# Optimization experiments

Measured on AMD Instinct MI355X. Metric: run time of the kernel, lower is better.

## Reference

```python
import jax, jax.numpy as jnp
import numpy as np

N_NODES = 10000
N_EDGES = 320000
ND, ED = 256, 128
CAT = 2 * ND + ED  # 640


def setup_inputs() -> dict:
    key = jax.random.key(0)
    ks = jax.random.split(key, 12)
    s = 0.05
    inp = {
        'node_attr': jax.random.normal(ks[0], (N_NODES, ND), jnp.float32),
        'edge_attr': jax.random.normal(ks[1], (N_EDGES, ED), jnp.float32),
        'edge_index': jax.random.randint(ks[2], (2, N_EDGES), 0, N_NODES, jnp.int32),
        'mw0': jax.random.normal(ks[3], (CAT, ND), jnp.float32) * s,
        'mb0': jnp.zeros((ND,), jnp.float32),
        'mw1': jax.random.normal(ks[4], (ND, ND), jnp.float32) * s,
        'mb1': jnp.zeros((ND,), jnp.float32),
        'mw2': jax.random.normal(ks[5], (ND, ND), jnp.float32) * s,
        'mb2': jnp.zeros((ND,), jnp.float32),
        'ew0': jax.random.normal(ks[6], (CAT, ED), jnp.float32) * s,
        'eb0': jnp.zeros((ED,), jnp.float32),
        'ew1': jax.random.normal(ks[7], (ED, ED), jnp.float32) * s,
        'eb1': jnp.zeros((ED,), jnp.float32),
        'ew2': jax.random.normal(ks[8], (ED, ED), jnp.float32) * s,
        'eb2': jnp.zeros((ED,), jnp.float32),
        'aw': jax.random.normal(ks[9], (CAT, 1), jnp.float32) * s,
        'ab': jnp.zeros((1,), jnp.float32),
    }
    return inp


def _mlp3(f, w0, b0, w1, b1, w2, b2):
    h = jax.nn.relu(f @ w0 + b0)
    h = jax.nn.relu(h @ w1 + b1)
    return h @ w2 + b2


def reference(node_attr, edge_attr, edge_index,
              mw0, mb0, mw1, mb1, mw2, mb2,
              ew0, eb0, ew1, eb1, ew2, eb2, aw, ab):
    n = node_attr.shape[0]
    src, dst = edge_index[0], edge_index[1]
    # [E, 2*ND+ED] gathered per-edge features
    feat = jnp.concatenate([node_attr[src], node_attr[dst], edge_attr], axis=-1)

    messages = _mlp3(feat, mw0, mb0, mw1, mb1, mw2, mb2)        # [E, ND]
    att = (feat @ aw + ab)[:, 0]                                 # [E]

    # scatter_softmax over edges grouped by source node (stable)
    seg_max = jax.ops.segment_max(att, src, num_segments=n)
    seg_max = jnp.where(jnp.isfinite(seg_max), seg_max, 0.0)     # empty segments
    ex = jnp.exp(att - seg_max[src])
    denom = jax.ops.segment_sum(ex, src, num_segments=n)
    alpha = ex / denom[src]                                      # [E]

    x_out = jax.ops.segment_sum(alpha[:, None] * messages, src, num_segments=n)  # [N, ND]
    e_out = _mlp3(feat, ew0, eb0, ew1, eb1, ew2, eb2)            # [E, ED]
    return x_out, e_out
```

## Files before the change

kernel.cpp:

```cpp
#include <hip/hip_runtime.h>
#include <hip/hip_bf16.h>

#define N_NODES 10000
#define E_EDGES 320000
#define ND 256
#define ED 128

#define B_AM   0
#define B_BM   5120000
#define B_AE   10240000
#define B_BE   12800000
#define B_P1   15360000
#define B_P2   15400960
#define B_XA   15441920
#define B_DEN  25681920
#define B_CNT  25722880
#define B_ROW  25763840
#define B_CUR  25804800
#define B_EID  25845760
#define B_WT   27125760

#define M0T 0
#define M1T 65536
#define M2T 196608
#define E0T 327680
#define E1T 360448
#define E2T 393216

#define R0 0
#define R1 16384
#define R2 32768
#define R3 49152
#define AL_S  65536
#define SRC_S 65792
#define DST_S 66048
#define EID_S 66304
#define LDS_TOT 66560

#define BM 64
#define NTILES (E_EDGES / BM)

typedef float  float4v __attribute__((ext_vector_type(4)));
typedef short  short8  __attribute__((ext_vector_type(8)));

__device__ __forceinline__ unsigned short f2bf(float f) {
    unsigned int b = __float_as_uint(f);
    return (unsigned short)((b + 0x7FFFu + ((b >> 16) & 1u)) >> 16);
}
__device__ __forceinline__ float bf2f(unsigned short u) {
    return __uint_as_float(((unsigned int)u) << 16);
}
__device__ __forceinline__ unsigned int pkbf(float a, float b) {
    __hip_bfloat162 h = __float22bfloat162_rn(float2{a, b});
    return *(unsigned int*)&h;
}

__device__ __forceinline__ void bar_ldsonly() {
    asm volatile("s_waitcnt lgkmcnt(0)" ::: "memory");
    __builtin_amdgcn_s_barrier();
}

__global__ void k_init(float* xa, float* den, int* cnt, int* cur) {
    int i = blockIdx.x * blockDim.x + threadIdx.x;
    int st = gridDim.x * blockDim.x;
    for (int j = i; j < N_NODES * ND; j += st) xa[j] = 0.f;
    for (int j = i; j < N_NODES; j += st) { den[j] = 0.f; cnt[j] = 0; cur[j] = 0; }
}

__global__ void k_deg(const int* ei, int* cnt) {
    int e = blockIdx.x * 256 + threadIdx.x;
    if (e < E_EDGES) atomicAdd(&cnt[ei[e]], 1);
}

__global__ __launch_bounds__(1024) void k_scan(const int* cnt, int* rowstart) {
    __shared__ int wsum[16];
    int t = threadIdx.x, lane = t & 63, w = t >> 6;
    int base = t * 10;
    int loc[10];
    int s = 0;
    #pragma unroll
    for (int i = 0; i < 10; i++) {
        int idx = base + i;
        int v = (idx < N_NODES) ? cnt[idx] : 0;
        loc[i] = s; s += v;
    }
    int run = s;
    #pragma unroll
    for (int d = 1; d < 64; d <<= 1) {
        int u = __shfl_up(run, d);
        if (lane >= d) run += u;
    }
    if (lane == 63) wsum[w] = run;
    __syncthreads();
    if (w == 0 && lane < 16) {
        int v = wsum[lane];
        int r = v;
        #pragma unroll
        for (int d = 1; d < 16; d <<= 1) {
            int u = __shfl_up(r, d);
            if (lane >= d) r += u;
        }
        wsum[lane] = r - v;
    }
    __syncthreads();
    int ex = wsum[w] + run - s;
    #pragma unroll
    for (int i = 0; i < 10; i++) {
        int idx = base + i;
        if (idx < N_NODES) rowstart[idx] = ex + loc[i];
    }
}

__global__ void k_fill(const int* ei, const int* rowstart, int* cur, int* eidcsr) {
    int e = blockIdx.x * 256 + threadIdx.x;
    if (e >= E_EDGES) return;
    int s = ei[e];
    int p = atomicAdd(&cur[s], 1);
    eidcsr[rowstart[s] + p] = e;
}

__global__ void k_wconv(const float* mw0, const float* mw1, const float* mw2,
                        const float* ew0, const float* ew1, const float* ew2, char* wtb) {
    const int tot = 212992;
    for (int idx = blockIdx.x * blockDim.x + threadIdx.x; idx < tot;
         idx += gridDim.x * blockDim.x) {
        int local, K, N, base; const float* src;
        if (idx < 32768)       { local = idx;          K = 128; N = 256; src = mw0 + 512*256; base = M0T; }
        else if (idx < 98304)  { local = idx - 32768;  K = 256; N = 256; src = mw1;           base = M1T; }
        else if (idx < 163840) { local = idx - 98304;  K = 256; N = 256; src = mw2;           base = M2T; }
        else if (idx < 180224) { local = idx - 163840; K = 128; N = 128; src = ew0 + 512*128; base = E0T; }
        else if (idx < 196608) { local = idx - 180224; K = 128; N = 128; src = ew1;           base = E1T; }
        else                   { local = idx - 196608; K = 128; N = 128; src = ew2;           base = E2T; }
        int W4 = N / 4;
        int CF = W4 >> 4;
        int NK = K / 32;
        int t = local;
        int j    = t & 7;   t >>= 3;
        int lane = t & 63;  t >>= 6;
        int cf   = t % CF;  t /= CF;
        int kk   = t % NK;  t /= NK;
        int wc   = t;
        int col = wc * W4 + cf * 16 + (lane & 15);
        int k   = kk * 32 + (lane >> 4) * 8 + j;
        ((unsigned short*)(wtb + base))[local] = f2bf(src[k * N + col]);
    }
}

__global__ __launch_bounds__(256) void k_nodepre(
    const float* na, const float* mw0, const float* ew0, const float* aw,
    const float* mb0, const float* eb0, const float* ab, char* wsb) {
    __shared__ float at[256 * 8];
    int tid = threadIdx.x;
    int r0 = blockIdx.x * 8;
    {
        int r = tid & 7, kq = tid >> 3;
        const float* src = na + (size_t)(r0 + r) * ND + kq * 8;
        float4 v0 = *(const float4*)(src);
        float4 v1 = *(const float4*)(src + 4);
        int kb = kq * 8;
        at[(kb+0)*8 + r] = v0.x; at[(kb+1)*8 + r] = v0.y;
        at[(kb+2)*8 + r] = v0.z; at[(kb+3)*8 + r] = v0.w;
        at[(kb+4)*8 + r] = v1.x; at[(kb+5)*8 + r] = v1.y;
        at[(kb+6)*8 + r] = v1.z; at[(kb+7)*8 + r] = v1.w;
    }
    __syncthreads();
    int c = blockIdx.y * 256 + tid;
    if (c >= 770) return;
    const float* wp; int wstep; float bias;
    unsigned short* opu = nullptr; float* opf = nullptr; int ostride;
    if (c < 256)      { wp = mw0 + c;                 wstep = 256; bias = mb0[c];     opu = (unsigned short*)(wsb + B_AM) + c;       ostride = 256; }
    else if (c < 512) { wp = mw0 + 65536 + (c - 256); wstep = 256; bias = 0.f;        opu = (unsigned short*)(wsb + B_BM) + (c-256); ostride = 256; }
    else if (c < 640) { wp = ew0 + (c - 512);         wstep = 128; bias = eb0[c-512]; opu = (unsigned short*)(wsb + B_AE) + (c-512); ostride = 128; }
    else if (c < 768) { wp = ew0 + 32768 + (c - 640); wstep = 128; bias = 0.f;        opu = (unsigned short*)(wsb + B_BE) + (c-640); ostride = 128; }
    else if (c == 768){ wp = aw;                      wstep = 1;   bias = ab[0];      opf = (float*)(wsb + B_P1);                    ostride = 1; }
    else              { wp = aw + 256;                wstep = 1;   bias = 0.f;        opf = (float*)(wsb + B_P2);                    ostride = 1; }
    float acc[8];
    #pragma unroll
    for (int r = 0; r < 8; r++) acc[r] = 0.f;
    for (int k = 0; k < 256; k++) {
        float w = wp[k * wstep];
        const float* a = &at[k * 8];
        float4 a0 = *(const float4*)(a);
        float4 a1 = *(const float4*)(a + 4);
        acc[0] += a0.x * w; acc[1] += a0.y * w; acc[2] += a0.z * w; acc[3] += a0.w * w;
        acc[4] += a1.x * w; acc[5] += a1.y * w; acc[6] += a1.z * w; acc[7] += a1.w * w;
    }
    if (opu) { for (int r = 0; r < 8; r++) opu[(size_t)(r0 + r) * ostride] = f2bf(acc[r] + bias); }
    else     { for (int r = 0; r < 8; r++) opf[(size_t)(r0 + r)] = acc[r] + bias; }
}

struct DP {
    const float* ea; const int* ei; const int* csr;
    const unsigned short* Am; const unsigned short* Bm;
    const unsigned short* Ae; const unsigned short* Be;
    const float* p1; const float* p2; const float* aw;
    const float* mb1; const float* mb2; const float* eb1; const float* eb2;
    const char* wtb;
    float* xa; float* den; float* eout;
};

__device__ __forceinline__ int pan_addr(int blo, int bhi, int row, int col) {
    int base = (col & 128) ? bhi : blo;
    return base + row * 256 + ((((col & 127)) * 2) ^ ((row & 7) << 4));
}
__device__ __forceinline__ int dump_addr(int row, int col) {
    return row * 1024 + (((col * 4)) ^ ((row & 15) << 6));
}

template<int KTOT, int NOUT, int EPI, int NXT_N>
__device__ __forceinline__ void do_gemm(char* sm, const DP& p,
                                        int a_lo, int a_hi, const char* wt,
                                        int h_lo, int h_hi, const float* bias,
                                        const char* wt_next, short8 (&bbuf)[2][4],
                                        int wr, int wc, int lane) {
    constexpr int WCOL = NOUT / 4;
    constexpr int CF   = WCOL / 16;
    constexpr int NK   = KTOT / 32;
    constexpr int KH   = NK * CF / 4;
    constexpr int NKH  = NK / KH;
    const int l15 = lane & 15, lg = lane >> 4;
    const float4v vz = {0.f, 0.f, 0.f, 0.f};
    float4v acc[2][CF];
    #pragma unroll
    for (int i = 0; i < 2; i++)
        #pragma unroll
        for (int j = 0; j < CF; j++) acc[i][j] = vz;
    bar_ldsonly();
    short8 areg[2][2];
    #pragma unroll
    for (int rf = 0; rf < 2; rf++)
        areg[0][rf] = *(const short8*)(sm + pan_addr(a_lo, a_hi, wr*32 + rf*16 + l15, lg*8));
    #pragma unroll
    for (int h = 0; h < KH; h++) {
        if (h + 1 < KH) {
            #pragma unroll
            for (int i = 0; i < 4; i++)
                bbuf[(h+1)&1][i] = *(const short8*)(wt + ((size_t)((h+1)*4 + i) * 64 + lane) * 16);
        } else if constexpr (NXT_N > 0) {
            #pragma unroll
            for (int i = 0; i < NXT_N; i++)
                bbuf[(h+1)&1][i] = *(const short8*)(wt_next + ((size_t)i * 64 + lane) * 16);
        }
        #pragma unroll
        for (int ks = 0; ks < NKH; ks++) {
            int kstep = h * NKH + ks;
            if (kstep + 1 < NK) {
                int ke = (kstep + 1) * 32 + lg * 8;
                #pragma unroll
                for (int rf = 0; rf < 2; rf++)
                    areg[(kstep+1)&1][rf] = *(const short8*)(sm + pan_addr(a_lo, a_hi, wr*32 + rf*16 + l15, ke));
            }
            #pragma unroll
            for (int rf = 0; rf < 2; rf++)
                #pragma unroll
                for (int cf = 0; cf < CF; cf++)
                    acc[rf][cf] = __builtin_amdgcn_mfma_f32_16x16x32_bf16(areg[kstep&1][rf], bbuf[h&1][ks*CF+cf], acc[rf][cf], 0, 0, 0);
        }
    }
    if constexpr (EPI == 2) bar_ldsonly();
    const int*   srcid = (const int*)(sm + SRC_S);
    const int*   dstid = (const int*)(sm + DST_S);
    const int*   eid   = (const int*)(sm + EID_S);
    const float* exv   = (const float*)(sm + AL_S);
    #pragma unroll
    for (int rf = 0; rf < 2; rf++)
        #pragma unroll
        for (int cf = 0; cf < CF; cf++) {
            int col = wc * WCOL + cf * 16 + l15;
            int row0 = wr * 32 + rf * 16 + lg * 4;
            if constexpr (EPI == 0 || EPI == 1 || EPI == 3) {
                float vv[4];
                #pragma unroll
                for (int j = 0; j < 4; j++) {
                    int row = row0 + j;
                    float v = acc[rf][cf][j];
                    if constexpr (EPI == 0)
                        v += bf2f(p.Am[(size_t)srcid[row] * ND + col]) + bf2f(p.Bm[(size_t)dstid[row] * ND + col]);
                    else if constexpr (EPI == 1)
                        v += bias[col];
                    else
                        v += bf2f(p.Ae[(size_t)srcid[row] * ED + col]) + bf2f(p.Be[(size_t)dstid[row] * ED + col]);
                    vv[j] = fmaxf(v, 0.f);
                }
                unsigned w01 = pkbf(vv[0], vv[1]);
                unsigned w23 = pkbf(vv[2], vv[3]);
                *(unsigned short*)(sm + pan_addr(h_lo, h_hi, row0 + 0, col)) = (unsigned short)w01;
                *(unsigned short*)(sm + pan_addr(h_lo, h_hi, row0 + 1, col)) = (unsigned short)(w01 >> 16);
                *(unsigned short*)(sm + pan_addr(h_lo, h_hi, row0 + 2, col)) = (unsigned short)w23;
                *(unsigned short*)(sm + pan_addr(h_lo, h_hi, row0 + 3, col)) = (unsigned short)(w23 >> 16);
            } else {
                #pragma unroll
                for (int j = 0; j < 4; j++) {
                    int row = row0 + j;
                    float v = acc[rf][cf][j];
                    if constexpr (EPI == 2) {
                        v = (v + p.mb2[col]) * exv[row];
                        *(float*)(sm + dump_addr(row, col)) = v;
                    } else {
                        v += p.eb2[col];
                        p.eout[(size_t)eid[row] * ED + col] = v;
                    }
                }
            }
        }
}

__global__ __launch_bounds__(512, 4) void k_main(DP p) {
    extern __shared__ char sm[];
    const int tid = threadIdx.x;
    const int lane = tid & 63, wv = tid >> 6;
    const int wr = wv >> 2, wc = wv & 3;
    const int s0 = blockIdx.x * BM;

    const char* wtE0 = p.wtb + E0T + (size_t)wc * 8192;
    const char* wtE1 = p.wtb + E1T + (size_t)wc * 8192;
    const char* wtE2 = p.wtb + E2T + (size_t)wc * 8192;
    const char* wtM0 = p.wtb + M0T + (size_t)wc * 16384;
    const char* wtM1 = p.wtb + M1T + (size_t)wc * 32768;
    const char* wtM2 = p.wtb + M2T + (size_t)wc * 32768;

    short8 bbuf[2][4];
    #pragma unroll
    for (int i = 0; i < 4; i++)
        bbuf[0][i] = *(const short8*)(wtE0 + ((size_t)i * 64 + lane) * 16);

    if (tid < BM) {
        int eid = p.csr[s0 + tid];
        ((int*)(sm + EID_S))[tid] = eid;
        ((int*)(sm + SRC_S))[tid] = p.ei[eid];
        ((int*)(sm + DST_S))[tid] = p.ei[E_EDGES + eid];
    }
    {
        int r = tid >> 3, cq = tid & 7;
        int eid = p.csr[s0 + r];
        const float4* src = (const float4*)(p.ea + (size_t)eid * ED + cq * 16);
        const float4* wvp = (const float4*)(p.aw + 512 + cq * 16);
        int s = (r & 7) << 4;
        float4 v0 = src[0], v1 = src[1], v2 = src[2], v3 = src[3];
        float4 w0 = wvp[0], w1 = wvp[1], w2 = wvp[2], w3 = wvp[3];
        float sd = v0.x*w0.x + v0.y*w0.y + v0.z*w0.z + v0.w*w0.w
                 + v1.x*w1.x + v1.y*w1.y + v1.z*w1.z + v1.w*w1.w
                 + v2.x*w2.x + v2.y*w2.y + v2.z*w2.z + v2.w*w2.w
                 + v3.x*w3.x + v3.y*w3.y + v3.z*w3.z + v3.w*w3.w;
        int cb = cq * 32;
        *(uint4*)(sm + R0 + r*256 + (cb ^ s)) =
            make_uint4(pkbf(v0.x,v0.y), pkbf(v0.z,v0.w), pkbf(v1.x,v1.y), pkbf(v1.z,v1.w));
        *(uint4*)(sm + R0 + r*256 + ((cb + 16) ^ s)) =
            make_uint4(pkbf(v2.x,v2.y), pkbf(v2.z,v2.w), pkbf(v3.x,v3.y), pkbf(v3.z,v3.w));
        sd += __shfl_xor(sd, 1); sd += __shfl_xor(sd, 2); sd += __shfl_xor(sd, 4);
        if (cq == 0) {
            int sn = p.ei[eid];
            int dn = p.ei[E_EDGES + eid];
            float a = sd + p.p1[sn] + p.p2[dn];
            float ex = __expf(a);
            ((float*)(sm + AL_S))[r] = ex;
            unsafeAtomicAdd(&p.den[sn], ex);
        }
    }
    do_gemm<128,128,3,4>(sm, p, R0, 0,  wtE0, R1, 0,  nullptr, wtE1, bbuf, wr, wc, lane);
    do_gemm<128,128,1,4>(sm, p, R1, 0,  wtE1, R2, 0,  p.eb1,   wtE2, bbuf, wr, wc, lane);
    do_gemm<128,128,4,4>(sm, p, R2, 0,  wtE2, 0,  0,  nullptr, wtM0, bbuf, wr, wc, lane);
    do_gemm<128,256,0,4>(sm, p, R0, 0,  wtM0, R1, R2, nullptr, wtM1, bbuf, wr, wc, lane);
    do_gemm<256,256,1,4>(sm, p, R1, R2, wtM1, R0, R3, p.mb1,   wtM2, bbuf, wr, wc, lane);
    do_gemm<256,256,2,0>(sm, p, R0, R3, wtM2, 0,  0,  nullptr, nullptr, bbuf, wr, wc, lane);
    bar_ldsonly();
    {
        const int* srcid = (const int*)(sm + SRC_S);
        int h = tid >> 8;
        int c = tid & 255;
        int rend = h * 32 + 31;
        float acc = 0.f;
        for (int r = h * 32; r <= rend; r++) {
            acc += *(const float*)(sm + dump_addr(r, c));
            if (r == rend || srcid[r + 1] != srcid[r]) {
                unsafeAtomicAdd(&p.xa[(size_t)srcid[r] * ND + c], acc);
                acc = 0.f;
            }
        }
    }
}

__global__ void k_norm(const float* xa, const float* den, float* xout) {
    int i = blockIdx.x * 256 + threadIdx.x;
    if (i >= N_NODES * ND) return;
    float d = den[i >> 8];
    xout[i] = (d > 0.f) ? xa[i] / d : 0.f;
}

extern "C" void kernel_launch(void* const* d_in, const int* in_sizes, int n_in,
                              void* d_out, int out_size, void* d_ws, size_t ws_size,
                              hipStream_t stream) {
    const float* na  = (const float*)d_in[0];
    const float* ea  = (const float*)d_in[1];
    const int*   ei  = (const int*)d_in[2];
    const float* mw0 = (const float*)d_in[3];
    const float* mb0 = (const float*)d_in[4];
    const float* mw1 = (const float*)d_in[5];
    const float* mb1 = (const float*)d_in[6];
    const float* mw2 = (const float*)d_in[7];
    const float* mb2 = (const float*)d_in[8];
    const float* ew0 = (const float*)d_in[9];
    const float* eb0 = (const float*)d_in[10];
    const float* ew1 = (const float*)d_in[11];
    const float* eb1 = (const float*)d_in[12];
    const float* ew2 = (const float*)d_in[13];
    const float* eb2 = (const float*)d_in[14];
    const float* aw  = (const float*)d_in[15];
    const float* ab  = (const float*)d_in[16];
    float* out = (float*)d_out;
    char*  wsb = (char*)d_ws;

    float* xout = out;
    float* eout = out + (size_t)N_NODES * ND;

    float* xa  = (float*)(wsb + B_XA);
    float* den = (float*)(wsb + B_DEN);
    int*   cnt = (int*)(wsb + B_CNT);
    int*   row = (int*)(wsb + B_ROW);
    int*   cur = (int*)(wsb + B_CUR);
    int*   eidcsr = (int*)(wsb + B_EID);

    k_init<<<512, 256, 0, stream>>>(xa, den, cnt, cur);
    k_deg<<<1250, 256, 0, stream>>>(ei, cnt);
    k_scan<<<1, 1024, 0, stream>>>(cnt, row);
    k_fill<<<1250, 256, 0, stream>>>(ei, row, cur, eidcsr);
    k_wconv<<<256, 256, 0, stream>>>(mw0, mw1, mw2, ew0, ew1, ew2, wsb + B_WT);
    k_nodepre<<<dim3(1250, 4), 256, 0, stream>>>(na, mw0, ew0, aw, mb0, eb0, ab, wsb);

    DP p{ea, ei, eidcsr,
         (const unsigned short*)(wsb + B_AM), (const unsigned short*)(wsb + B_BM),
         (const unsigned short*)(wsb + B_AE), (const unsigned short*)(wsb + B_BE),
         (const float*)(wsb + B_P1), (const float*)(wsb + B_P2), aw,
         mb1, mb2, eb1, eb2, (const char*)(wsb + B_WT), xa, den, eout};
    hipFuncSetAttribute((const void*)k_main, hipFuncAttributeMaxDynamicSharedMemorySize, LDS_TOT);
    k_main<<<NTILES, 512, LDS_TOT, stream>>>(p);
    k_norm<<<10000, 256, 0, stream>>>(xa, den, xout);
}
```

Baseline: 503.5 us.

## Replace scalar node precompute with bf16 MFMA GEMM and separate attention dot kernel

The per-node projection of node features through the src/dst slices of the first message and edge MLP layers now runs as a bf16 MFMA GEMM over 64-node tiles, using weights pre-swizzled by the weight-conversion kernel. Previously it was a scalar FP32 loop reading weights from global memory with strided access. The two attention projections move to a small shuffle-reduction kernel. This trades FP32 precision for bf16 inputs in the projection and adds an extra kernel launch.

```diff
diff --git a/kernel.cpp b/kernel.cpp
--- a/kernel.cpp
+++ b/kernel.cpp
@@ -26,6 +26,8 @@
 #define E0T 327680
 #define E1T 360448
 #define E2T 393216
+#define NPT0 425984
+#define NPSEC 65536
 
 #define R0 0
 #define R1 16384
@@ -121,72 +123,173 @@
 
 __global__ void k_wconv(const float* mw0, const float* mw1, const float* mw2,
                         const float* ew0, const float* ew1, const float* ew2, char* wtb) {
-    const int tot = 212992;
+    const int tot = 409600;
     for (int idx = blockIdx.x * blockDim.x + threadIdx.x; idx < tot;
          idx += gridDim.x * blockDim.x) {
-        int local, K, N, base; const float* src;
-        if (idx < 32768)       { local = idx;          K = 128; N = 256; src = mw0 + 512*256; base = M0T; }
-        else if (idx < 98304)  { local = idx - 32768;  K = 256; N = 256; src = mw1;           base = M1T; }
-        else if (idx < 163840) { local = idx - 98304;  K = 256; N = 256; src = mw2;           base = M2T; }
-        else if (idx < 180224) { local = idx - 163840; K = 128; N = 128; src = ew0 + 512*128; base = E0T; }
-        else if (idx < 196608) { local = idx - 180224; K = 128; N = 128; src = ew1;           base = E1T; }
-        else                   { local = idx - 196608; K = 128; N = 128; src = ew2;           base = E2T; }
-        int W4 = N / 4;
-        int CF = W4 >> 4;
-        int NK = K / 32;
-        int t = local;
-        int j    = t & 7;   t >>= 3;
-        int lane = t & 63;  t >>= 6;
-        int cf   = t % CF;  t /= CF;
-        int kk   = t % NK;  t /= NK;
-        int wc   = t;
-        int col = wc * W4 + cf * 16 + (lane & 15);
-        int k   = kk * 32 + (lane >> 4) * 8 + j;
-        ((unsigned short*)(wtb + base))[local] = f2bf(src[k * N + col]);
-    }
-}
-
-__global__ __launch_bounds__(256) void k_nodepre(
-    const float* na, const float* mw0, const float* ew0, const float* aw,
-    const float* mb0, const float* eb0, const float* ab, char* wsb) {
-    __shared__ float at[256 * 8];
-    int tid = threadIdx.x;
-    int r0 = blockIdx.x * 8;
+        if (idx < 212992) {
+            int local, K, N, base; const float* src;
+            if (idx < 32768)       { local = idx;          K = 128; N = 256; src = mw0 + 512*256; base = M0T; }
+            else if (idx < 98304)  { local = idx - 32768;  K = 256; N = 256; src = mw1;           base = M1T; }
+            else if (idx < 163840) { local = idx - 98304;  K = 256; N = 256; src = mw2;           base = M2T; }
+            else if (idx < 180224) { local = idx - 163840; K = 128; N = 128; src = ew0 + 512*128; base = E0T; }
+            else if (idx < 196608) { local = idx - 180224; K = 128; N = 128; src = ew1;           base = E1T; }
+            else                   { local = idx - 196608; K = 128; N = 128; src = ew2;           base = E2T; }
+            int W4 = N / 4;
+            int CF = W4 >> 4;
+            int NK = K / 32;
+            int t = local;
+            int j    = t & 7;   t >>= 3;
+            int lane = t & 63;  t >>= 6;
+            int cf   = t % CF;  t /= CF;
+            int kk   = t % NK;  t /= NK;
+            int wc   = t;
+            int col = wc * W4 + cf * 16 + (lane & 15);
+            int k   = kk * 32 + (lane >> 4) * 8 + j;
+            ((unsigned short*)(wtb + base))[local] = f2bf(src[k * N + col]);
+        } else {
+            int q = idx - 212992;
+            int sec = q >> 15;
+            int local = q & 32767;
+            int t = local;
+            int j    = t & 7;   t >>= 3;
+            int lane = t & 63;  t >>= 6;
+            int cf   = t & 1;   t >>= 1;
+            int kk   = t & 7;   t >>= 3;
+            int wc   = t;
+            int col = wc * 32 + cf * 16 + (lane & 15);
+            int k   = kk * 32 + (lane >> 4) * 8 + j;
+            const float* src; int N;
+            if (sec == 0)      { src = mw0;         N = 256; }
+            else if (sec == 1) { src = mw0;         N = 256; col += 128; }
+            else if (sec == 2) { src = mw0 + 65536; N = 256; }
+            else if (sec == 3) { src = mw0 + 65536; N = 256; col += 128; }
+            else if (sec == 4) { src = ew0;         N = 128; }
+            else               { src = ew0 + 32768; N = 128; }
+            ((unsigned short*)(wtb + NPT0 + sec * NPSEC))[local] = f2bf(src[k * N + col]);
+        }
+    }
+}
+
+__device__ __forceinline__ int np_addr(int row, int keb) {
+    return row * 512 + (keb ^ ((row & 7) << 4));
+}
+
+__global__ __launch_bounds__(512, 2) void k_npgemm(const float* na, const float* mb0,
+                                                   const float* eb0, char* wsb) {
+    __shared__ char sm[32768];
+    const int tid = threadIdx.x;
+    const int lane = tid & 63, wv = tid >> 6;
+    const int wr = wv >> 2, wc = wv & 3;
+    const int l15 = lane & 15, lg = lane >> 4;
+    const int n0 = blockIdx.x * 64;
+    const int sec = blockIdx.y;
+
+    const char* wt = wsb + B_WT + NPT0 + (size_t)sec * NPSEC + (size_t)wc * 16384;
+    short8 bbuf[2][4];
+    #pragma unroll
+    for (int i = 0; i < 4; i++)
+        bbuf[0][i] = *(const short8*)(wt + ((size_t)i * 64 + lane) * 16);
+
     {
-        int r = tid & 7, kq = tid >> 3;
-        const float* src = na + (size_t)(r0 + r) * ND + kq * 8;
-        float4 v0 = *(const float4*)(src);
-        float4 v1 = *(const float4*)(src + 4);
-        int kb = kq * 8;
-        at[(kb+0)*8 + r] = v0.x; at[(kb+1)*8 + r] = v0.y;
-        at[(kb+2)*8 + r] = v0.z; at[(kb+3)*8 + r] = v0.w;
-        at[(kb+4)*8 + r] = v1.x; at[(kb+5)*8 + r] = v1.y;
-        at[(kb+6)*8 + r] = v1.z; at[(kb+7)*8 + r] = v1.w;
-    }
-    __syncthreads();
-    int c = blockIdx.y * 256 + tid;
-    if (c >= 770) return;
-    const float* wp; int wstep; float bias;
-    unsigned short* opu = nullptr; float* opf = nullptr; int ostride;
-    if (c < 256)      { wp = mw0 + c;                 wstep = 256; bias = mb0[c];     opu = (unsigned short*)(wsb + B_AM) + c;       ostride = 256; }
-    else if (c < 512) { wp = mw0 + 65536 + (c - 256); wstep = 256; bias = 0.f;        opu = (unsigned short*)(wsb + B_BM) + (c-256); ostride = 256; }
-    else if (c < 640) { wp = ew0 + (c - 512);         wstep = 128; bias = eb0[c-512]; opu = (unsigned short*)(wsb + B_AE) + (c-512); ostride = 128; }
-    else if (c < 768) { wp = ew0 + 32768 + (c - 640); wstep = 128; bias = 0.f;        opu = (unsigned short*)(wsb + B_BE) + (c-640); ostride = 128; }
-    else if (c == 768){ wp = aw;                      wstep = 1;   bias = ab[0];      opf = (float*)(wsb + B_P1);                    ostride = 1; }
-    else              { wp = aw + 256;                wstep = 1;   bias = 0.f;        opf = (float*)(wsb + B_P2);                    ostride = 1; }
-    float acc[8];
-    #pragma unroll
-    for (int r = 0; r < 8; r++) acc[r] = 0.f;
-    for (int k = 0; k < 256; k++) {
-        float w = wp[k * wstep];
-        const float* a = &at[k * 8];
-        float4 a0 = *(const float4*)(a);
-        float4 a1 = *(const float4*)(a + 4);
-        acc[0] += a0.x * w; acc[1] += a0.y * w; acc[2] += a0.z * w; acc[3] += a0.w * w;
-        acc[4] += a1.x * w; acc[5] += a1.y * w; acc[6] += a1.z * w; acc[7] += a1.w * w;
-    }
-    if (opu) { for (int r = 0; r < 8; r++) opu[(size_t)(r0 + r) * ostride] = f2bf(acc[r] + bias); }
-    else     { for (int r = 0; r < 8; r++) opf[(size_t)(r0 + r)] = acc[r] + bias; }
+        int r = tid >> 3, cq = tid & 7;
+        int node = n0 + r;
+        int sxor = (r & 7) << 4;
+        if (node < N_NODES) {
+            const float4* src = (const float4*)(na + (size_t)node * ND + cq * 32);
+            #pragma unroll
+            for (int g = 0; g < 4; g++) {
+                float4 va = src[g*2], vb = src[g*2+1];
+                uint4 pk = make_uint4(pkbf(va.x,va.y), pkbf(va.z,va.w),
+                                      pkbf(vb.x,vb.y), pkbf(vb.z,vb.w));
+                *(uint4*)(sm + np_addr(r, (cq*32 + g*8)*2)) = pk;
+            }
+        } else {
+            #pragma unroll
+            for (int g = 0; g < 4; g++)
+                *(uint4*)(sm + np_addr(r, (cq*32 + g*8)*2)) = make_uint4(0,0,0,0);
+        }
+    }
+    bar_ldsonly();
+
+    const float4v vz = {0.f, 0.f, 0.f, 0.f};
+    float4v acc[2][2];
+    #pragma unroll
+    for (int i = 0; i < 2; i++) { acc[i][0] = vz; acc[i][1] = vz; }
+
+    short8 areg[2][2];
+    #pragma unroll
+    for (int rf = 0; rf < 2; rf++)
+        areg[0][rf] = *(const short8*)(sm + np_addr(wr*32 + rf*16 + l15, lg*16));
+
+    #pragma unroll
+    for (int h = 0; h < 4; h++) {
+        if (h + 1 < 4) {
+            #pragma unroll
+            for (int i = 0; i < 4; i++)
+                bbuf[(h+1)&1][i] = *(const short8*)(wt + ((size_t)((h+1)*4 + i) * 64 + lane) * 16);
+        }
+        #pragma unroll
+        for (int ks = 0; ks < 2; ks++) {
+            int kstep = h * 2 + ks;
+            if (kstep + 1 < 8) {
+                int keb = (kstep + 1) * 64 + lg * 16;
+                #pragma unroll
+                for (int rf = 0; rf < 2; rf++)
+                    areg[(kstep+1)&1][rf] = *(const short8*)(sm + np_addr(wr*32 + rf*16 + l15, keb));
+            }
+            #pragma unroll
+            for (int rf = 0; rf < 2; rf++)
+                #pragma unroll
+                for (int cf = 0; cf < 2; cf++)
+                    acc[rf][cf] = __builtin_amdgcn_mfma_f32_16x16x32_bf16(areg[kstep&1][rf], bbuf[h&1][ks*2+cf], acc[rf][cf], 0, 0, 0);
+        }
+    }
+    const float* bias = nullptr;
+    unsigned short* outp; int ostride; int coladd = 0;
+    if (sec == 0)      { outp = (unsigned short*)(wsb + B_AM); ostride = 256; bias = mb0; }
+    else if (sec == 1) { outp = (unsigned short*)(wsb + B_AM); ostride = 256; bias = mb0 + 128; coladd = 128; }
+    else if (sec == 2) { outp = (unsigned short*)(wsb + B_BM); ostride = 256; }
+    else if (sec == 3) { outp = (unsigned short*)(wsb + B_BM); ostride = 256; coladd = 128; }
+    else if (sec == 4) { outp = (unsigned short*)(wsb + B_AE); ostride = 128; bias = eb0; }
+    else               { outp = (unsigned short*)(wsb + B_BE); ostride = 128; }
+    #pragma unroll
+    for (int rf = 0; rf < 2; rf++)
+        #pragma unroll
+        for (int cf = 0; cf < 2; cf++) {
+            int colLoc = wc * 32 + cf * 16 + l15;
+            float b = bias ? bias[colLoc] : 0.f;
+            #pragma unroll
+            for (int j = 0; j < 4; j++) {
+                int node = n0 + wr*32 + rf*16 + lg*4 + j;
+                if (node < N_NODES)
+                    outp[(size_t)node * ostride + coladd + colLoc] = f2bf(acc[rf][cf][j] + b);
+            }
+        }
+}
+
+__global__ __launch_bounds__(256) void k_p1p2(const float* na, const float* aw,
+                                              const float* ab, char* wsb) {
+    int t = blockIdx.x * 256 + threadIdx.x;
+    int node = t >> 4, kc = t & 15;
+    if (node >= N_NODES) return;
+    const float4* row = (const float4*)(na + (size_t)node * ND + kc * 16);
+    const float4* w1p = (const float4*)(aw + kc * 16);
+    const float4* w2p = (const float4*)(aw + 256 + kc * 16);
+    float s1 = 0.f, s2 = 0.f;
+    #pragma unroll
+    for (int i = 0; i < 4; i++) {
+        float4 v = row[i], w1 = w1p[i], w2 = w2p[i];
+        s1 += v.x*w1.x + v.y*w1.y + v.z*w1.z + v.w*w1.w;
+        s2 += v.x*w2.x + v.y*w2.y + v.z*w2.z + v.w*w2.w;
+    }
+    s1 += __shfl_xor(s1, 1); s1 += __shfl_xor(s1, 2);
+    s1 += __shfl_xor(s1, 4); s1 += __shfl_xor(s1, 8);
+    s2 += __shfl_xor(s2, 1); s2 += __shfl_xor(s2, 2);
+    s2 += __shfl_xor(s2, 4); s2 += __shfl_xor(s2, 8);
+    if (kc == 0) {
+        ((float*)(wsb + B_P1))[node] = s1 + ab[0];
+        ((float*)(wsb + B_P2))[node] = s2;
+    }
 }
 
 struct DP {
@@ -424,8 +527,9 @@
     k_deg<<<1250, 256, 0, stream>>>(ei, cnt);
     k_scan<<<1, 1024, 0, stream>>>(cnt, row);
     k_fill<<<1250, 256, 0, stream>>>(ei, row, cur, eidcsr);
-    k_wconv<<<256, 256, 0, stream>>>(mw0, mw1, mw2, ew0, ew1, ew2, wsb + B_WT);
-    k_nodepre<<<dim3(1250, 4), 256, 0, stream>>>(na, mw0, ew0, aw, mb0, eb0, ab, wsb);
+    k_wconv<<<400, 256, 0, stream>>>(mw0, mw1, mw2, ew0, ew1, ew2, wsb + B_WT);
+    k_npgemm<<<dim3(157, 6), 512, 0, stream>>>(na, mb0, eb0, wsb);
+    k_p1p2<<<625, 256, 0, stream>>>(na, aw, ab, wsb);
 
     DP p{ea, ei, eidcsr,
          (const unsigned short*)(wsb + B_AM), (const unsigned short*)(wsb + B_BM),
```

After: 443.8 us. 11.9% less time.
